# Performance work log

Hardware: AMD Instinct MI355X
Metric: run time of the kernel (lower is better)

Reference implementation:

```python
import jax, jax.numpy as jnp
import numpy as np

CLASSES = 11  # log2 tile values 0..10
B = 262144


def setup_inputs() -> dict:
    key = jax.random.key(0)
    k1, k2, k3 = jax.random.split(key, 3)
    # boards: 0 (empty) or powers of 2 up to 2^10, per the 2048 game / classes=11
    e = jax.random.randint(k1, (B, 4, 4), 0, CLASSES)
    x = jnp.where(e == 0, 0.0, jnp.exp2(e.astype(jnp.float32)))
    W0 = jax.random.normal(k2, (4, CLASSES + 1, 1, 2), dtype=jnp.float32) * 0.1
    b0 = jnp.full((4,), 0.01, dtype=jnp.float32)
    W1 = jax.random.normal(k3, (4, CLASSES + 1, 2, 1), dtype=jnp.float32) * 0.1
    return {"x": x, "W0": W0, "b0": b0, "W1": W1}


def _preprocess(x):
    # x: [B,4,4] raw tile values
    corners = jnp.stack([x[:, 0, 0], x[:, 0, -1], x[:, -1, 0], x[:, -1, -1]], axis=1)
    ix = jnp.argmax(corners, axis=1)
    fv = (ix // 2) == 1  # vertical flip (rows)
    fh = (ix % 2) == 1   # horizontal flip (cols)
    x = jnp.where(fv[:, None, None], x[:, ::-1, :], x)
    x = jnp.where(fh[:, None, None], x[:, :, ::-1], x)
    xlog = jnp.log2(x + (x == 0)).astype(jnp.int32)           # [B,4,4] in 0..10
    onehot = jax.nn.one_hot(xlog, CLASSES, dtype=jnp.float32)  # [B,4,4,11]
    out = jnp.transpose(onehot, (0, 3, 1, 2))                  # [B,11,4,4]
    mask = out.sum(axis=1, keepdims=True)                      # occupancy mask
    out = jnp.concatenate([mask, out], axis=1)                 # [B,12,4,4]
    # unscramble: undo flip-dependent channel ordering (vert swaps 0<->1, horiz swaps 2<->3)
    perm_v = jnp.array([1, 0, 2, 3, 4, 5, 6, 7, 8, 9, 10, 11])
    perm_h = jnp.array([0, 1, 3, 2, 4, 5, 6, 7, 8, 9, 10, 11])
    out = jnp.where(fv[:, None, None, None], out[:, perm_v], out)
    out = jnp.where(fh[:, None, None, None], out[:, perm_h], out)
    return out


def _conv(x, W):
    return jax.lax.conv_general_dilated(
        x, W, window_strides=(1, 1), padding='VALID',
        dimension_numbers=('NCHW', 'OIHW', 'NCHW'))


def reference(x, W0, b0, W1):
    p = _preprocess(x)                                   # [B,12,4,4]
    zh = jax.nn.relu(_conv(p, W0) + b0[None, :, None, None])  # [B,4,4,3]
    zv = jax.nn.relu(_conv(p, W1))                             # [B,4,3,4]
    # transpose zv so the horizontal/vertical feature maps can be stacked
    return jnp.stack((zh, jnp.transpose(zv, (0, 1, 3, 2))), axis=1)  # [B,2,4,4,3]
```

## Files before the change

### kernel.cpp

```cpp
#include <hip/hip_runtime.h>


__device__ __forceinline__ int chmap(int e, int fv, int fh) {
    if (e == 0) return fv ? 0 : 1;
    if (e == 1) return fh ? 3 : 2;
    if (e == 2) return fh ? 2 : 3;
    return 1 + e;
}

__global__ __launch_bounds__(1024) void smartcnn_kernel(
    const float* __restrict__ x,
    const float* __restrict__ W0,
    const float* __restrict__ b0,
    const float* __restrict__ W1,
    float* __restrict__ out,
    int B)
{
    __shared__ float tabH[1936];
    __shared__ float tabV[1936];
    __shared__ float sW0[96], sW1[96], sb0[4];

    const int t = threadIdx.x;
    if (t < 96) { sW0[t] = W0[t]; sW1[t] = W1[t]; }
    if (t < 4)  sb0[t] = b0[t];
    __syncthreads();

#pragma unroll
    for (int it = 0; it < 2; ++it) {
        int id = t + it * 1024;
        if (id < 1936) {
            int e2 = id % 11;
            int r  = id / 11;
            int e1 = r % 11;
            int fo = r / 11;
            int o = fo & 3, flip = fo >> 2;
            int fvv = flip >> 1, fhh = flip & 1;
            int ch1 = chmap(e1, fvv, fhh);
            int ch2 = chmap(e2, fvv, fhh);
            int mc2 = fvv ? 2 : 0;
            int o24 = o * 24;
            float C0 = sb0[o] + sW0[o24 + mc2] + sW0[o24 + mc2 + 1];
            float C1 =          sW1[o24 + mc2] + sW1[o24 + mc2 + 1];
            tabH[id] = fmaxf(C0 + sW0[o24 + ch1 * 2] + sW0[o24 + ch2 * 2 + 1], 0.0f);
            tabV[id] = fmaxf(C1 + sW1[o24 + ch1 * 2] + sW1[o24 + ch2 * 2 + 1], 0.0f);
        }
    }
    __syncthreads();

    const int gq = blockIdx.x * 1024 + t;
    const int b = gq >> 2;
    const int q = gq & 3;
    if (b >= B) return;

    float4 row = ((const float4*)x)[(size_t)b * 4 + q];

#define EV(v) (max((int)(__float_as_uint(v) >> 23) - 127, 0))
    unsigned my = (unsigned)EV(row.x)        | ((unsigned)EV(row.y) << 4) |
                  ((unsigned)EV(row.z) << 8) | ((unsigned)EV(row.w) << 12);
#undef EV
    unsigned oth1 = __shfl_xor(my, 1);
    unsigned pair = (q & 1) ? ((my << 16) | oth1) : ((oth1 << 16) | my);
    unsigned oth2 = __shfl_xor(pair, 2);
    unsigned pk0 = (q & 2) ? oth2 : pair;
    unsigned pk1 = (q & 2) ? pair : oth2;

    int e00 = pk0 & 15, e03 = (pk0 >> 12) & 15;
    int e30 = (pk1 >> 16) & 15, e33 = (int)(pk1 >> 28);
    int best = e00, ix = 0;
    if (e03 > best) { best = e03; ix = 1; }
    if (e30 > best) { best = e30; ix = 2; }
    if (e33 > best) { best = e33; ix = 3; }
    const int fv = ix >> 1, fh = ix & 1;

    unsigned fva = (pk1 >> 16) | (pk1 << 16);
    unsigned fvb = (pk0 >> 16) | (pk0 << 16);
    pk0 = fv ? fva : pk0;
    pk1 = fv ? fvb : pk1;
    unsigned ra = ((pk0 & 0x0F0F0F0Fu) << 4) | ((pk0 >> 4) & 0x0F0F0F0Fu);
    ra = ((ra & 0x00FF00FFu) << 8) | ((ra >> 8) & 0x00FF00FFu);
    unsigned rb = ((pk1 & 0x0F0F0F0Fu) << 4) | ((pk1 >> 4) & 0x0F0F0F0Fu);
    rb = ((rb & 0x00FF00FFu) << 8) | ((rb >> 8) & 0x00FF00FFu);
    pk0 = fh ? ra : pk0;
    pk1 = fh ? rb : pk1;

    const unsigned long long pk = ((unsigned long long)pk1 << 32) | (unsigned long long)pk0;
#define EX(c) ((int)((pk >> ((c) * 4)) & 15ull))

    float4* out4 = (float4*)out + (size_t)b * 24;

#pragma unroll
    for (int rp = 0; rp < 3; ++rp) {
        int n = rp * 4 + q;
        int o = (n * 11) >> 5;
        int s = n - 3 * o;
        int f1 = (s == 2) ? 1 : 0;
        int f2 = (s >= 1) ? 1 : 0;
        int s5 = s * 5;
        int base = (ix * 4 + o) * 121;

        int c0 = s5, c1 = s5 + 1 + f1, c2 = s5 + 2 + f2, c3 = s5 + 4;
        float4 vh;
        vh.x = tabH[base + EX(c0) * 11 + EX(c0 + 1)];
        vh.y = tabH[base + EX(c1) * 11 + EX(c1 + 1)];
        vh.z = tabH[base + EX(c2) * 11 + EX(c2 + 1)];
        vh.w = tabH[base + EX(c3) * 11 + EX(c3 + 1)];
        out4[rp * 4 + q] = vh;

        int d0 = s5, d1 = s5 + 4 - 11 * f1, d2 = s5 + 8 - 11 * f2, d3 = s5 + 1;
        float4 vv;
        vv.x = tabV[base + EX(d0) * 11 + EX(d0 + 4)];
        vv.y = tabV[base + EX(d1) * 11 + EX(d1 + 4)];
        vv.z = tabV[base + EX(d2) * 11 + EX(d2 + 4)];
        vv.w = tabV[base + EX(d3) * 11 + EX(d3 + 4)];
        out4[12 + rp * 4 + q] = vv;
    }
#undef EX
}

extern "C" void kernel_launch(void* const* d_in, const int* in_sizes, int n_in,
                              void* d_out, int out_size, void* d_ws, size_t ws_size,
                              hipStream_t stream) {
    const float* x  = (const float*)d_in[0];
    const float* W0 = (const float*)d_in[1];
    const float* b0 = (const float*)d_in[2];
    const float* W1 = (const float*)d_in[3];
    float* out = (float*)d_out;

    int B = in_sizes[0] / 16;
    int total = B * 4;
    int blocks = (total + 1023) / 1024;
    smartcnn_kernel<<<blocks, 1024, 0, stream>>>(x, W0, b0, W1, out, B);
}
```

Baseline: 25.01 us.

## Use grid-stride loop with 256-thread blocks and drop shuffle-based board assembly

Launches a capped grid of 256-thread blocks that loop over quads, so each block's lookup-table build is reused across several iterations. Each thread now loads all four rows of its board directly instead of assembling them through warp shuffles. This trades shuffle instructions for four-times-redundant global loads that rely on cache hits, and smaller blocks need more loop iterations of table build per block.

```diff
diff --git a/kernel.cpp b/kernel.cpp
--- a/kernel.cpp
+++ b/kernel.cpp
@@ -8,13 +8,13 @@
     return 1 + e;
 }
 
-__global__ __launch_bounds__(1024) void smartcnn_kernel(
+__global__ __launch_bounds__(256) void smartcnn_kernel(
     const float* __restrict__ x,
     const float* __restrict__ W0,
     const float* __restrict__ b0,
     const float* __restrict__ W1,
     float* __restrict__ out,
-    int B)
+    int nquads)
 {
     __shared__ float tabH[1936];
     __shared__ float tabV[1936];
@@ -26,8 +26,8 @@
     __syncthreads();
 
 #pragma unroll
-    for (int it = 0; it < 2; ++it) {
-        int id = t + it * 1024;
+    for (int k = 0; k < 8; ++k) {
+        int id = t + k * 256;
         if (id < 1936) {
             int e2 = id % 11;
             int r  = id / 11;
@@ -47,74 +47,78 @@
     }
     __syncthreads();
 
-    const int gq = blockIdx.x * 1024 + t;
-    const int b = gq >> 2;
-    const int q = gq & 3;
-    if (b >= B) return;
+    const int stride = gridDim.x * 256;
+    for (int gq = blockIdx.x * 256 + t; gq < nquads; gq += stride) {
+        const int b = gq >> 2;
+        const int q = gq & 3;
 
-    float4 row = ((const float4*)x)[(size_t)b * 4 + q];
+        const float4* x4 = (const float4*)x + (size_t)b * 4;
+        float4 r0 = x4[0], r1 = x4[1], r2 = x4[2], r3 = x4[3];
 
 #define EV(v) (max((int)(__float_as_uint(v) >> 23) - 127, 0))
-    unsigned my = (unsigned)EV(row.x)        | ((unsigned)EV(row.y) << 4) |
-                  ((unsigned)EV(row.z) << 8) | ((unsigned)EV(row.w) << 12);
+        unsigned pk0 = (unsigned)EV(r0.x)        | ((unsigned)EV(r0.y) << 4)  |
+                       ((unsigned)EV(r0.z) << 8)  | ((unsigned)EV(r0.w) << 12) |
+                       ((unsigned)EV(r1.x) << 16) | ((unsigned)EV(r1.y) << 20) |
+                       ((unsigned)EV(r1.z) << 24) | ((unsigned)EV(r1.w) << 28);
+        unsigned pk1 = (unsigned)EV(r2.x)        | ((unsigned)EV(r2.y) << 4)  |
+                       ((unsigned)EV(r2.z) << 8)  | ((unsigned)EV(r2.w) << 12) |
+                       ((unsigned)EV(r3.x) << 16) | ((unsigned)EV(r3.y) << 20) |
+                       ((unsigned)EV(r3.z) << 24) | ((unsigned)EV(r3.w) << 28);
 #undef EV
-    unsigned oth1 = __shfl_xor(my, 1);
-    unsigned pair = (q & 1) ? ((my << 16) | oth1) : ((oth1 << 16) | my);
-    unsigned oth2 = __shfl_xor(pair, 2);
-    unsigned pk0 = (q & 2) ? oth2 : pair;
-    unsigned pk1 = (q & 2) ? pair : oth2;
 
-    int e00 = pk0 & 15, e03 = (pk0 >> 12) & 15;
-    int e30 = (pk1 >> 16) & 15, e33 = (int)(pk1 >> 28);
-    int best = e00, ix = 0;
-    if (e03 > best) { best = e03; ix = 1; }
-    if (e30 > best) { best = e30; ix = 2; }
-    if (e33 > best) { best = e33; ix = 3; }
-    const int fv = ix >> 1, fh = ix & 1;
+        int e00 = pk0 & 15, e03 = (pk0 >> 12) & 15;
+        int e30 = (pk1 >> 16) & 15, e33 = (int)(pk1 >> 28);
+        int best = e00, ix = 0;
+        if (e03 > best) { best = e03; ix = 1; }
+        if (e30 > best) { best = e30; ix = 2; }
+        if (e33 > best) { best = e33; ix = 3; }
+        const int fv = ix >> 1, fh = ix & 1;
 
-    unsigned fva = (pk1 >> 16) | (pk1 << 16);
-    unsigned fvb = (pk0 >> 16) | (pk0 << 16);
-    pk0 = fv ? fva : pk0;
-    pk1 = fv ? fvb : pk1;
-    unsigned ra = ((pk0 & 0x0F0F0F0Fu) << 4) | ((pk0 >> 4) & 0x0F0F0F0Fu);
-    ra = ((ra & 0x00FF00FFu) << 8) | ((ra >> 8) & 0x00FF00FFu);
-    unsigned rb = ((pk1 & 0x0F0F0F0Fu) << 4) | ((pk1 >> 4) & 0x0F0F0F0Fu);
-    rb = ((rb & 0x00FF00FFu) << 8) | ((rb >> 8) & 0x00FF00FFu);
-    pk0 = fh ? ra : pk0;
-    pk1 = fh ? rb : pk1;
+        unsigned fva = (pk1 >> 16) | (pk1 << 16);
+        unsigned fvb = (pk0 >> 16) | (pk0 << 16);
+        pk0 = fv ? fva : pk0;
+        pk1 = fv ? fvb : pk1;
+        unsigned ra = ((pk0 & 0x0F0F0F0Fu) << 4) | ((pk0 >> 4) & 0x0F0F0F0Fu);
+        ra = ((ra & 0x00FF00FFu) << 8) | ((ra >> 8) & 0x00FF00FFu);
+        unsigned rb = ((pk1 & 0x0F0F0F0Fu) << 4) | ((pk1 >> 4) & 0x0F0F0F0Fu);
+        rb = ((rb & 0x00FF00FFu) << 8) | ((rb >> 8) & 0x00FF00FFu);
+        pk0 = fh ? ra : pk0;
+        pk1 = fh ? rb : pk1;
 
-    const unsigned long long pk = ((unsigned long long)pk1 << 32) | (unsigned long long)pk0;
+        const unsigned long long pk =
+            ((unsigned long long)pk1 << 32) | (unsigned long long)pk0;
 #define EX(c) ((int)((pk >> ((c) * 4)) & 15ull))
 
-    float4* out4 = (float4*)out + (size_t)b * 24;
+        float4* out4 = (float4*)out + (size_t)b * 24;
 
 #pragma unroll
-    for (int rp = 0; rp < 3; ++rp) {
-        int n = rp * 4 + q;
-        int o = (n * 11) >> 5;
-        int s = n - 3 * o;
-        int f1 = (s == 2) ? 1 : 0;
-        int f2 = (s >= 1) ? 1 : 0;
-        int s5 = s * 5;
-        int base = (ix * 4 + o) * 121;
+        for (int rp = 0; rp < 3; ++rp) {
+            int n = rp * 4 + q;
+            int o = (n * 11) >> 5;
+            int s = n - 3 * o;
+            int f1 = (s == 2) ? 1 : 0;
+            int f2 = (s >= 1) ? 1 : 0;
+            int s5 = s * 5;
+            int base = (ix * 4 + o) * 121;
 
-        int c0 = s5, c1 = s5 + 1 + f1, c2 = s5 + 2 + f2, c3 = s5 + 4;
-        float4 vh;
-        vh.x = tabH[base + EX(c0) * 11 + EX(c0 + 1)];
-        vh.y = tabH[base + EX(c1) * 11 + EX(c1 + 1)];
-        vh.z = tabH[base + EX(c2) * 11 + EX(c2 + 1)];
-        vh.w = tabH[base + EX(c3) * 11 + EX(c3 + 1)];
-        out4[rp * 4 + q] = vh;
+            int c0 = s5, c1 = s5 + 1 + f1, c2 = s5 + 2 + f2, c3 = s5 + 4;
+            float4 vh;
+            vh.x = tabH[base + EX(c0) * 11 + EX(c0 + 1)];
+            vh.y = tabH[base + EX(c1) * 11 + EX(c1 + 1)];
+            vh.z = tabH[base + EX(c2) * 11 + EX(c2 + 1)];
+            vh.w = tabH[base + EX(c3) * 11 + EX(c3 + 1)];
+            out4[rp * 4 + q] = vh;
 
-        int d0 = s5, d1 = s5 + 4 - 11 * f1, d2 = s5 + 8 - 11 * f2, d3 = s5 + 1;
-        float4 vv;
-        vv.x = tabV[base + EX(d0) * 11 + EX(d0 + 4)];
-        vv.y = tabV[base + EX(d1) * 11 + EX(d1 + 4)];
-        vv.z = tabV[base + EX(d2) * 11 + EX(d2 + 4)];
-        vv.w = tabV[base + EX(d3) * 11 + EX(d3 + 4)];
-        out4[12 + rp * 4 + q] = vv;
+            int d0 = s5, d1 = s5 + 4 - 11 * f1, d2 = s5 + 8 - 11 * f2, d3 = s5 + 1;
+            float4 vv;
+            vv.x = tabV[base + EX(d0) * 11 + EX(d0 + 4)];
+            vv.y = tabV[base + EX(d1) * 11 + EX(d1 + 4)];
+            vv.z = tabV[base + EX(d2) * 11 + EX(d2 + 4)];
+            vv.w = tabV[base + EX(d3) * 11 + EX(d3 + 4)];
+            out4[12 + rp * 4 + q] = vv;
+        }
+#undef EX
     }
-#undef EX
 }
 
 extern "C" void kernel_launch(void* const* d_in, const int* in_sizes, int n_in,
@@ -127,7 +131,9 @@
     float* out = (float*)d_out;
 
     int B = in_sizes[0] / 16;
-    int total = B * 4;
-    int blocks = (total + 1023) / 1024;
-    smartcnn_kernel<<<blocks, 1024, 0, stream>>>(x, W0, b0, W1, out, B);
+    int nquads = B * 4;
+    int blocks = 2048;
+    int need = (nquads + 255) / 256;
+    if (blocks > need) blocks = need;
+    smartcnn_kernel<<<blocks, 256, 0, stream>>>(x, W0, b0, W1, out, nquads);
 }
```

After: 28.42 us. 1.14x slower.
